# Kernel optimization log

Hardware: AMD Instinct MI355X
Metric: run time of the kernel (lower is better)

## Reference

```python
import jax, jax.numpy as jnp
import numpy as np

N_NODES = 100000
N_EDGES = 1600000
HIDDEN = 128
N_GRAPHS = 64
N_CLASSES = 10


def setup_inputs() -> dict:
    key = jax.random.key(0)
    ks = jax.random.split(key, 10)
    x = jax.random.normal(ks[0], (N_NODES, 1), dtype=jnp.float32)
    edge_index = jax.random.randint(ks[1], (2, N_EDGES), 0, N_NODES, dtype=jnp.int32)
    batch = jnp.sort(jax.random.randint(ks[2], (N_NODES,), 0, N_GRAPHS, dtype=jnp.int32))
    def glorot(k, shape):
        fan_in, fan_out = shape
        s = jnp.sqrt(6.0 / (fan_in + fan_out))
        return jax.random.uniform(k, shape, jnp.float32, -s, s)
    return {
        "x": x,
        "edge_index": edge_index,
        "batch": batch,
        "W1l": glorot(ks[3], (1, HIDDEN)),
        "W1r": glorot(ks[4], (1, HIDDEN)),
        "b1": jnp.zeros((HIDDEN,), jnp.float32),
        "W2l": glorot(ks[5], (HIDDEN, HIDDEN)),
        "W2r": glorot(ks[6], (HIDDEN, HIDDEN)),
        "b2": jnp.zeros((HIDDEN,), jnp.float32),
        "W3l": glorot(ks[7], (HIDDEN, HIDDEN)),
        "W3r": glorot(ks[8], (HIDDEN, HIDDEN)),
        "b3": jnp.zeros((HIDDEN,), jnp.float32),
        "Wfc": glorot(ks[9], (HIDDEN, N_CLASSES)),
        "bfc": jnp.zeros((N_CLASSES,), jnp.float32),
    }


def _sage_conv(x, src, dst, Wl, Wr, b, n_nodes):
    # mean aggregation of source features at destination nodes
    msg = x[src]                                              # [E, d_in]
    agg = jax.ops.segment_sum(msg, dst, num_segments=n_nodes)  # [N, d_in]
    cnt = jax.ops.segment_sum(jnp.ones((src.shape[0], 1), x.dtype), dst,
                              num_segments=n_nodes)            # [N, 1]
    mean = agg / jnp.maximum(cnt, 1.0)
    # PyG SAGEConv: lin_l(mean neighbors) + bias + lin_r(self)
    return mean @ Wl + b + x @ Wr


def reference(x, edge_index, batch, W1l, W1r, b1, W2l, W2r, b2,
              W3l, W3r, b3, Wfc, bfc):
    src, dst = edge_index[0], edge_index[1]
    n = x.shape[0]
    h = jax.nn.relu(_sage_conv(x, src, dst, W1l, W1r, b1, n))
    h = jax.nn.relu(_sage_conv(h, src, dst, W2l, W2r, b2, n))
    h = jax.nn.relu(_sage_conv(h, src, dst, W3l, W3r, b3, n))
    # global_mean_pool over graph ids in `batch`
    pooled = jax.ops.segment_sum(h, batch, num_segments=N_GRAPHS)
    gcnt = jax.ops.segment_sum(jnp.ones((n, 1), h.dtype), batch,
                               num_segments=N_GRAPHS)
    pooled = pooled / jnp.maximum(gcnt, 1.0)
    logits = pooled @ Wfc + bfc
    return jax.nn.log_softmax(logits, axis=1)
```

## Files before the change

kernel.cpp:

```cpp
#include <hip/hip_runtime.h>

typedef unsigned int u32;
typedef unsigned short u16;
typedef short bf16x8 __attribute__((ext_vector_type(8)));
typedef float f32x4 __attribute__((ext_vector_type(4)));
typedef float f32x2 __attribute__((ext_vector_type(2)));
typedef u32 u32x4 __attribute__((ext_vector_type(4)));

#define HBLK 256

__device__ __forceinline__ u16 f2bf(float f) {
  u32 u = __float_as_uint(f);
  u = (u + 0x7FFFu + ((u >> 16) & 1u)) >> 16;
  return (u16)u;
}
__device__ __forceinline__ float bf2f(u32 h) { return __uint_as_float(h << 16); }

__global__ void hist_wprep_kernel(const int* __restrict__ dst, int* __restrict__ hist,
                                  int E, int nbuk, int chunk,
                                  const float* __restrict__ W2l, const float* __restrict__ W2r,
                                  const float* __restrict__ W3l, const float* __restrict__ W3r,
                                  u16* __restrict__ wt2, u16* __restrict__ wt3,
                                  float* __restrict__ pooled, int* __restrict__ gcnt) {
  int idx = blockIdx.x * 256 + threadIdx.x;
  {
    int which = idx >> 15, r = idx & 32767;
    int j = r >> 8, k = r & 255;
    if (which == 0) {
      float v = (k < 128) ? W2l[k * 128 + j] : W2r[(k - 128) * 128 + j];
      wt2[r] = f2bf(v);
    } else {
      float v = (k < 128) ? W3l[k * 128 + j] : W3r[(k - 128) * 128 + j];
      wt3[r] = f2bf(v);
    }
    if (idx < 8192) pooled[idx] = 0.f;
    if (idx < 64) gcnt[idx] = 0;
  }
  __shared__ int h[1024];
  for (int i = threadIdx.x; i < nbuk; i += 256) h[i] = 0;
  __syncthreads();
  int b0 = blockIdx.x * chunk, b1 = min(b0 + chunk, E);
  for (int e = b0 + threadIdx.x; e < b1; e += 256)
    atomicAdd(&h[dst[e] >> 7], 1);
  __syncthreads();
  for (int i = threadIdx.x; i < nbuk; i += 256)
    hist[i * HBLK + blockIdx.x] = h[i];
}

__global__ void scan_local(const int* __restrict__ in, int* __restrict__ out,
                           int* __restrict__ bsum, int n) {
  __shared__ int s[256];
  int tid = threadIdx.x;
  int i = blockIdx.x * 256 + tid;
  int v = (i < n) ? in[i] : 0;
  s[tid] = v;
  __syncthreads();
  for (int off = 1; off < 256; off <<= 1) {
    int t = (tid >= off) ? s[tid - off] : 0;
    __syncthreads();
    s[tid] += t;
    __syncthreads();
  }
  if (i < n) out[i] = s[tid] - v;
  if (tid == 255) bsum[blockIdx.x] = s[255];
}

__global__ void scan_fix(int* __restrict__ a, const int* __restrict__ bsum, int n,
                         int* __restrict__ bbase) {
  __shared__ int red[256];
  int tid = threadIdx.x, b = blockIdx.x;
  int s = 0;
  for (int k = tid; k < b; k += 256) s += bsum[k];
  red[tid] = s;
  __syncthreads();
  for (int off = 128; off; off >>= 1) {
    if (tid < off) red[tid] += red[tid + off];
    __syncthreads();
  }
  int i = b * 256 + tid;
  if (i < n) {
    int v = a[i] + red[0];
    a[i] = v;
    if (tid == 0) bbase[b] = v;
  }
}

__global__ void scatter2_kernel(const int* __restrict__ src, const int* __restrict__ dst,
                                const int* __restrict__ hist_s, u32* __restrict__ part,
                                int E, int nbuk, int chunk) {
  __shared__ int cur[1024];
  for (int i = threadIdx.x; i < nbuk; i += 256)
    cur[i] = hist_s[i * HBLK + blockIdx.x];
  __syncthreads();
  int b0 = blockIdx.x * chunk, b1 = min(b0 + chunk, E);
  for (int e = b0 + threadIdx.x; e < b1; e += 256) {
    int d = dst[e];
    int pos = atomicAdd(&cur[d >> 7], 1);
    part[pos] = (u32)src[e] | ((u32)(d & 127) << 25);
  }
}

__global__ void scatter3_kernel(const u32* __restrict__ part, const int* __restrict__ bbase,
                                const float* __restrict__ x,
                                const float* __restrict__ W1l, const float* __restrict__ W1r,
                                const float* __restrict__ b1,
                                int* __restrict__ roff, int* __restrict__ csr,
                                u32* __restrict__ h1, int E, int nbuk, int n) {
  int b = blockIdx.x;
  int tid = threadIdx.x;
  int base = bbase[b];
  int end = (b + 1 < nbuk) ? bbase[b + 1] : E;
  __shared__ int cnt[128];
  __shared__ int s[128];
  __shared__ int cur[128];
  __shared__ float xsum[128];
  __shared__ float meanv[128];
  __shared__ float wlA[128], wrA[128], bA[128];
  if (tid < 128) {
    cnt[tid] = 0; xsum[tid] = 0.f;
    wlA[tid] = W1l[tid]; wrA[tid] = W1r[tid]; bA[tid] = b1[tid];
  }
  __syncthreads();
  for (int e = base + tid; e < end; e += 256)
    atomicAdd(&cnt[part[e] >> 25], 1);
  __syncthreads();
  if (tid < 128) s[tid] = cnt[tid];
  __syncthreads();
  for (int off = 1; off < 128; off <<= 1) {
    int t = (tid >= off && tid < 128) ? s[tid - off] : 0;
    __syncthreads();
    if (tid < 128) s[tid] += t;
    __syncthreads();
  }
  if (tid < 128) {
    int excl = s[tid] - cnt[tid];
    cur[tid] = base + excl;
    int node = b * 128 + tid;
    if (node < n) roff[node] = base + excl;
  }
  if (b == 0 && tid == 0) roff[n] = E;
  __syncthreads();
  for (int e = base + tid; e < end; e += 256) {
    u32 p = part[e];
    int sidx = (int)(p & 0x1FFFFFFu);
    int pos = atomicAdd(&cur[p >> 25], 1);
    csr[pos] = sidx;
    atomicAdd(&xsum[p >> 25], x[sidx]);
  }
  __syncthreads();
  if (tid < 128) meanv[tid] = xsum[tid] / (float)max(cnt[tid], 1);
  __syncthreads();
  int nlocal = min(128, n - b * 128);
  for (int q = tid; q < nlocal * 64; q += 256) {
    int ln = q >> 6, w = q & 63;
    int node = b * 128 + ln;
    int j0 = w * 2;
    float m = meanv[ln], xs = x[node];
    float v0 = fmaxf(m * wlA[j0] + xs * wrA[j0] + bA[j0], 0.f);
    float v1 = fmaxf(m * wlA[j0 + 1] + xs * wrA[j0 + 1] + bA[j0 + 1], 0.f);
    h1[(size_t)node * 64 + w] = (u32)f2bf(v0) | ((u32)f2bf(v1) << 16);
  }
}

__global__ void agg_kernel(const int* __restrict__ csr, const int* __restrict__ roff,
                           const u32* __restrict__ hin, u32* __restrict__ outv, int n) {
  int wave = threadIdx.x >> 6, lane = threadIdx.x & 63;
  int i = blockIdx.x * 4 + wave;
  if (i >= n) return;
  int grp = lane >> 4, li = lane & 15;
  int e0 = roff[i], e1 = roff[i + 1];
  f32x2 a[4] = {};
  int e = e0 + grp;
  for (; e + 12 < e1; e += 16) {
    int s0 = csr[e], s1 = csr[e + 4], s2 = csr[e + 8], s3 = csr[e + 12];
    u32x4 v0 = *(const u32x4*)(hin + (size_t)s0 * 64 + li * 4);
    u32x4 v1 = *(const u32x4*)(hin + (size_t)s1 * 64 + li * 4);
    u32x4 v2 = *(const u32x4*)(hin + (size_t)s2 * 64 + li * 4);
    u32x4 v3 = *(const u32x4*)(hin + (size_t)s3 * 64 + li * 4);
#pragma unroll
    for (int w = 0; w < 4; ++w) {
      a[w] += (f32x2){bf2f(v0[w] & 0xFFFFu), bf2f(v0[w] >> 16)};
      a[w] += (f32x2){bf2f(v1[w] & 0xFFFFu), bf2f(v1[w] >> 16)};
      a[w] += (f32x2){bf2f(v2[w] & 0xFFFFu), bf2f(v2[w] >> 16)};
      a[w] += (f32x2){bf2f(v3[w] & 0xFFFFu), bf2f(v3[w] >> 16)};
    }
  }
  for (; e + 4 < e1; e += 8) {
    int s0 = csr[e], s1 = csr[e + 4];
    u32x4 v0 = *(const u32x4*)(hin + (size_t)s0 * 64 + li * 4);
    u32x4 v1 = *(const u32x4*)(hin + (size_t)s1 * 64 + li * 4);
#pragma unroll
    for (int w = 0; w < 4; ++w) {
      a[w] += (f32x2){bf2f(v0[w] & 0xFFFFu), bf2f(v0[w] >> 16)};
      a[w] += (f32x2){bf2f(v1[w] & 0xFFFFu), bf2f(v1[w] >> 16)};
    }
  }
  if (e < e1) {
    int s0 = csr[e];
    u32x4 v0 = *(const u32x4*)(hin + (size_t)s0 * 64 + li * 4);
#pragma unroll
    for (int w = 0; w < 4; ++w)
      a[w] += (f32x2){bf2f(v0[w] & 0xFFFFu), bf2f(v0[w] >> 16)};
  }
#pragma unroll
  for (int w = 0; w < 4; ++w) {
    a[w].x += __shfl_xor(a[w].x, 16, 64);
    a[w].y += __shfl_xor(a[w].y, 16, 64);
    a[w].x += __shfl_xor(a[w].x, 32, 64);
    a[w].y += __shfl_xor(a[w].y, 32, 64);
  }
  if (grp == 0) {
    float inv = 1.f / (float)max(e1 - e0, 1);
    u32x4 o;
#pragma unroll
    for (int w = 0; w < 4; ++w)
      o[w] = (u32)f2bf(a[w].x * inv) | ((u32)f2bf(a[w].y * inv) << 16);
    *(u32x4*)(outv + (size_t)i * 64 + li * 4) = o;
  }
}

__launch_bounds__(512)
__global__ void mm_kernel(const u16* Aleft, const u16* Aright,
                          const u16* __restrict__ Wt, const float* __restrict__ bias,
                          u16* Out, int n) {
  __shared__ u16 wlds[32768];
  for (int c = threadIdx.x; c < 4096; c += 512) {
    int j = c >> 5, ch = c & 31;
    int swz = ch ^ (j & 31);
    *(u32x4*)(&wlds[j * 256 + swz * 8]) = *(const u32x4*)(&Wt[j * 256 + ch * 8]);
  }
  __syncthreads();
  int wave = threadIdx.x >> 6;
  int lane = threadIdx.x & 63;
  int quad = lane >> 4, l16 = lane & 15;
  int row0 = blockIdx.x * 128 + wave * 16;
  int m = row0 + l16;
  int mc = m < n ? m : (n - 1);
  f32x4 acc[8] = {};
  const u16* Ah[2] = {Aleft, Aright};
#pragma unroll
  for (int half = 0; half < 2; ++half) {
    const u16* A = Ah[half] + (size_t)mc * 128;
#pragma unroll
    for (int s = 0; s < 4; ++s) {
      bf16x8 a = *(const bf16x8*)(A + s * 32 + quad * 8);
      int chunk = (half << 4) + (s << 2) + quad;
#pragma unroll
      for (int t = 0; t < 8; ++t) {
        int j = t * 16 + l16;
        int swz = chunk ^ (j & 31);
        bf16x8 b = *(const bf16x8*)(&wlds[j * 256 + swz * 8]);
        acc[t] = __builtin_amdgcn_mfma_f32_16x16x32_bf16(a, b, acc[t], 0, 0, 0);
      }
    }
  }
#pragma unroll
  for (int t = 0; t < 8; ++t) {
    int j = t * 16 + l16;
    float bj = bias[j];
#pragma unroll
    for (int r = 0; r < 4; ++r) {
      int mr = row0 + quad * 4 + r;
      if (mr < n) {
        float v = acc[t][r] + bj;
        Out[(size_t)mr * 128 + j] = f2bf(fmaxf(v, 0.f));
      }
    }
  }
}

#define PB_NODES 128
__global__ void pool_partial(const int* __restrict__ batch, const u32* __restrict__ h3,
                             float* __restrict__ pooled, int* __restrict__ gcnt, int n) {
  __shared__ int bg[PB_NODES];
  int tid = threadIdx.x;
  int start = blockIdx.x * PB_NODES;
  int cntN = min(PB_NODES, n - start);
  if (tid < cntN) bg[tid] = batch[start + tid];
  __syncthreads();
  int wave = tid >> 6, lane = tid & 63;
  float a0 = 0.f, a1 = 0.f;
  int gcur = -1, cnt = 0;
  int k = wave;
  for (; k + 12 < cntN; k += 16) {
    u32 v0 = h3[(size_t)(start + k) * 64 + lane];
    u32 v1 = h3[(size_t)(start + k + 4) * 64 + lane];
    u32 v2 = h3[(size_t)(start + k + 8) * 64 + lane];
    u32 v3 = h3[(size_t)(start + k + 12) * 64 + lane];
    int g0 = bg[k], g1 = bg[k + 4], g2 = bg[k + 8], g3 = bg[k + 12];
    u32 vv[4] = {v0, v1, v2, v3};
    int gg[4] = {g0, g1, g2, g3};
#pragma unroll
    for (int q = 0; q < 4; ++q) {
      if (gg[q] != gcur) {
        if (gcur >= 0) {
          atomicAdd(&pooled[gcur * 128 + lane * 2], a0);
          atomicAdd(&pooled[gcur * 128 + lane * 2 + 1], a1);
          if (lane == 0) atomicAdd(&gcnt[gcur], cnt);
        }
        gcur = gg[q]; a0 = 0.f; a1 = 0.f; cnt = 0;
      }
      a0 += bf2f(vv[q] & 0xFFFFu);
      a1 += bf2f(vv[q] >> 16);
      cnt++;
    }
  }
  for (; k < cntN; k += 4) {
    u32 v = h3[(size_t)(start + k) * 64 + lane];
    int g = bg[k];
    if (g != gcur) {
      if (gcur >= 0) {
        atomicAdd(&pooled[gcur * 128 + lane * 2], a0);
        atomicAdd(&pooled[gcur * 128 + lane * 2 + 1], a1);
        if (lane == 0) atomicAdd(&gcnt[gcur], cnt);
      }
      gcur = g; a0 = 0.f; a1 = 0.f; cnt = 0;
    }
    a0 += bf2f(v & 0xFFFFu);
    a1 += bf2f(v >> 16);
    cnt++;
  }
  if (gcur >= 0) {
    atomicAdd(&pooled[gcur * 128 + lane * 2], a0);
    atomicAdd(&pooled[gcur * 128 + lane * 2 + 1], a1);
    if (lane == 0) atomicAdd(&gcnt[gcur], cnt);
  }
}

__global__ void head_kernel(const float* __restrict__ pooled, const int* __restrict__ gcnt,
                            const float* __restrict__ Wfc, const float* __restrict__ bfc,
                            float* __restrict__ out) {
  __shared__ float lg[64][10];
  int t = threadIdx.x;
  if (t < 640) {
    int g = t / 10, c = t % 10;
    float inv = 1.f / (float)max(gcnt[g], 1);
    float acc = bfc[c];
    for (int k = 0; k < 128; ++k) acc += pooled[g * 128 + k] * inv * Wfc[k * 10 + c];
    lg[g][c] = acc;
  }
  __syncthreads();
  if (t < 640) {
    int g = t / 10, c = t % 10;
    float mx = -1e30f;
    for (int q = 0; q < 10; ++q) mx = fmaxf(mx, lg[g][q]);
    float se = 0.f;
    for (int q = 0; q < 10; ++q) se += expf(lg[g][q] - mx);
    out[g * 10 + c] = lg[g][c] - mx - logf(se);
  }
}

extern "C" void kernel_launch(void* const* d_in, const int* in_sizes, int n_in,
                              void* d_out, int out_size, void* d_ws, size_t ws_size,
                              hipStream_t stream) {
  const float* x   = (const float*)d_in[0];
  const int* ei    = (const int*)d_in[1];
  const int* batch = (const int*)d_in[2];
  const float* W1l = (const float*)d_in[3];
  const float* W1r = (const float*)d_in[4];
  const float* b1  = (const float*)d_in[5];
  const float* W2l = (const float*)d_in[6];
  const float* W2r = (const float*)d_in[7];
  const float* b2  = (const float*)d_in[8];
  const float* W3l = (const float*)d_in[9];
  const float* W3r = (const float*)d_in[10];
  const float* b3  = (const float*)d_in[11];
  const float* Wfc = (const float*)d_in[12];
  const float* bfc = (const float*)d_in[13];
  float* out = (float*)d_out;
  int N = in_sizes[0];
  int E = in_sizes[1] / 2;
  const int* src = ei;
  const int* dst = ei + E;

  char* p = (char*)d_ws;
  auto alloc = [&](size_t bytes) { void* r = (void*)p; p += (bytes + 255) & ~(size_t)255; return r; };
  int* roff   = (int*)alloc((size_t)(N + 1) * 4);
  int* csr    = (int*)alloc((size_t)E * 4);
  u32* bufA   = (u32*)alloc((size_t)N * 64 * 4);
  u32* bufB   = (u32*)alloc((size_t)N * 64 * 4);
  u16* wt2    = (u16*)alloc(32768 * 2);
  u16* wt3    = (u16*)alloc(32768 * 2);
  float* pooled = (float*)alloc(64 * 128 * 4);
  int* gcnt   = (int*)alloc(64 * 4);
  int* bsum   = (int*)alloc(1024 * 4);
  int* bbase  = (int*)alloc(1024 * 4);

  int nbuk = (N + 127) >> 7;
  int* hist = (int*)bufA;
  u32* part = (u32*)bufB;
  int chunk = (E + HBLK - 1) / HBLK;
  int nH = nbuk * HBLK;
  int nbH = (nH + 255) / 256;

  hist_wprep_kernel<<<HBLK, 256, 0, stream>>>(dst, hist, E, nbuk, chunk,
                                              W2l, W2r, W3l, W3r, wt2, wt3,
                                              pooled, gcnt);
  scan_local<<<nbH, 256, 0, stream>>>(hist, hist, bsum, nH);
  scan_fix<<<nbH, 256, 0, stream>>>(hist, bsum, nH, bbase);
  scatter2_kernel<<<HBLK, 256, 0, stream>>>(src, dst, hist, part, E, nbuk, chunk);
  scatter3_kernel<<<nbuk, 256, 0, stream>>>(part, bbase, x, W1l, W1r, b1,
                                            roff, csr, bufA, E, nbuk, N);
  agg_kernel<<<(N + 3) / 4, 256, 0, stream>>>(csr, roff, bufA, bufB, N);
  mm_kernel<<<(N + 127) / 128, 512, 0, stream>>>((const u16*)bufB, (const u16*)bufA, wt2, b2, (u16*)bufB, N);
  agg_kernel<<<(N + 3) / 4, 256, 0, stream>>>(csr, roff, bufB, bufA, N);
  mm_kernel<<<(N + 127) / 128, 512, 0, stream>>>((const u16*)bufA, (const u16*)bufB, wt3, b3, (u16*)bufA, N);
  pool_partial<<<(N + PB_NODES - 1) / PB_NODES, 256, 0, stream>>>(batch, bufA, pooled, gcnt, N);
  head_kernel<<<1, 640, 0, stream>>>(pooled, gcnt, Wfc, bfc, out);
}
```

Measured before the change: 346.0 us.

## Replace scan kernels with atomic bucket offsets and fuse pooling into final matmul

The two-pass global scan over the per-block histogram is removed. Each block now claims its bucket offset with an atomicAdd on per-bucket totals, and scatter2 computes the exclusive scan over the roughly 800 bucket totals itself in shared memory. The mean-pool partial reduction moves into the tail of the last mm_kernel, which reads back its freshly written output tile. This cuts three launches and one extra pass over h3, in exchange for a memset, a nondeterministic edge order inside each bucket, and a pooling loop that is no longer unrolled.

New measurement: 359.8 us. 1.04x slower.

```diff
diff --git a/kernel.cpp b/kernel.cpp
--- a/kernel.cpp
+++ b/kernel.cpp
@@ -16,8 +16,8 @@
 }
 __device__ __forceinline__ float bf2f(u32 h) { return __uint_as_float(h << 16); }
 
-__global__ void hist_wprep_kernel(const int* __restrict__ dst, int* __restrict__ hist,
-                                  int E, int nbuk, int chunk,
+__global__ void hist_wprep_kernel(const int* __restrict__ dst, int* __restrict__ boff,
+                                  int* __restrict__ btotal, int E, int nbuk, int chunk,
                                   const float* __restrict__ W2l, const float* __restrict__ W2r,
                                   const float* __restrict__ W3l, const float* __restrict__ W3r,
                                   u16* __restrict__ wt2, u16* __restrict__ wt3,
@@ -44,56 +44,44 @@
     atomicAdd(&h[dst[e] >> 7], 1);
   __syncthreads();
   for (int i = threadIdx.x; i < nbuk; i += 256)
-    hist[i * HBLK + blockIdx.x] = h[i];
-}
-
-__global__ void scan_local(const int* __restrict__ in, int* __restrict__ out,
-                           int* __restrict__ bsum, int n) {
-  __shared__ int s[256];
+    boff[i * HBLK + blockIdx.x] = atomicAdd(&btotal[i], h[i]);
+}
+
+__global__ void scatter2_kernel(const int* __restrict__ src, const int* __restrict__ dst,
+                                const int* __restrict__ btotal, const int* __restrict__ boff,
+                                u32* __restrict__ part, int* __restrict__ bbase,
+                                int E, int nbuk, int chunk) {
+  __shared__ int bt[1024];
+  __shared__ int wsum[256];
+  __shared__ int cur[1024];
   int tid = threadIdx.x;
-  int i = blockIdx.x * 256 + tid;
-  int v = (i < n) ? in[i] : 0;
-  s[tid] = v;
+  int t4 = tid * 4;
+  int v0 = (t4 + 0 < nbuk) ? btotal[t4 + 0] : 0;
+  int v1 = (t4 + 1 < nbuk) ? btotal[t4 + 1] : 0;
+  int v2 = (t4 + 2 < nbuk) ? btotal[t4 + 2] : 0;
+  int v3 = (t4 + 3 < nbuk) ? btotal[t4 + 3] : 0;
+  int sum = v0 + v1 + v2 + v3;
+  wsum[tid] = sum;
   __syncthreads();
   for (int off = 1; off < 256; off <<= 1) {
-    int t = (tid >= off) ? s[tid - off] : 0;
+    int t = (tid >= off) ? wsum[tid - off] : 0;
     __syncthreads();
-    s[tid] += t;
+    wsum[tid] += t;
     __syncthreads();
   }
-  if (i < n) out[i] = s[tid] - v;
-  if (tid == 255) bsum[blockIdx.x] = s[255];
-}
-
-__global__ void scan_fix(int* __restrict__ a, const int* __restrict__ bsum, int n,
-                         int* __restrict__ bbase) {
-  __shared__ int red[256];
-  int tid = threadIdx.x, b = blockIdx.x;
-  int s = 0;
-  for (int k = tid; k < b; k += 256) s += bsum[k];
-  red[tid] = s;
-  __syncthreads();
-  for (int off = 128; off; off >>= 1) {
-    if (tid < off) red[tid] += red[tid + off];
-    __syncthreads();
-  }
-  int i = b * 256 + tid;
-  if (i < n) {
-    int v = a[i] + red[0];
-    a[i] = v;
-    if (tid == 0) bbase[b] = v;
-  }
-}
-
-__global__ void scatter2_kernel(const int* __restrict__ src, const int* __restrict__ dst,
-                                const int* __restrict__ hist_s, u32* __restrict__ part,
-                                int E, int nbuk, int chunk) {
-  __shared__ int cur[1024];
-  for (int i = threadIdx.x; i < nbuk; i += 256)
-    cur[i] = hist_s[i * HBLK + blockIdx.x];
+  int excl = wsum[tid] - sum;
+  bt[t4 + 0] = excl;
+  bt[t4 + 1] = excl + v0;
+  bt[t4 + 2] = excl + v0 + v1;
+  bt[t4 + 3] = excl + v0 + v1 + v2;
+  __syncthreads();
+  for (int i = tid; i < nbuk; i += 256) {
+    cur[i] = bt[i] + boff[i * HBLK + blockIdx.x];
+    if (blockIdx.x == 0) bbase[i] = bt[i];
+  }
   __syncthreads();
   int b0 = blockIdx.x * chunk, b1 = min(b0 + chunk, E);
-  for (int e = b0 + threadIdx.x; e < b1; e += 256) {
+  for (int e = b0 + tid; e < b1; e += 256) {
     int d = dst[e];
     int pos = atomicAdd(&cur[d >> 7], 1);
     part[pos] = (u32)src[e] | ((u32)(d & 127) << 25);
@@ -222,8 +210,11 @@
 __launch_bounds__(512)
 __global__ void mm_kernel(const u16* Aleft, const u16* Aright,
                           const u16* __restrict__ Wt, const float* __restrict__ bias,
-                          u16* Out, int n) {
+                          u16* Out, int n,
+                          const int* __restrict__ batch, float* __restrict__ pooled,
+                          int* __restrict__ gcnt, int doPool) {
   __shared__ u16 wlds[32768];
+  __shared__ int bg[128];
   for (int c = threadIdx.x; c < 4096; c += 512) {
     int j = c >> 5, ch = c & 31;
     int swz = ch ^ (j & 31);
@@ -267,46 +258,17 @@
       }
     }
   }
-}
-
-#define PB_NODES 128
-__global__ void pool_partial(const int* __restrict__ batch, const u32* __restrict__ h3,
-                             float* __restrict__ pooled, int* __restrict__ gcnt, int n) {
-  __shared__ int bg[PB_NODES];
-  int tid = threadIdx.x;
-  int start = blockIdx.x * PB_NODES;
-  int cntN = min(PB_NODES, n - start);
-  if (tid < cntN) bg[tid] = batch[start + tid];
-  __syncthreads();
-  int wave = tid >> 6, lane = tid & 63;
+  if (!doPool) return;
+  __syncthreads();
+  int start = blockIdx.x * 128;
+  int cntN = min(128, n - start);
+  if (threadIdx.x < cntN) bg[threadIdx.x] = batch[start + threadIdx.x];
+  __syncthreads();
+  const u32* O32 = (const u32*)Out;
   float a0 = 0.f, a1 = 0.f;
   int gcur = -1, cnt = 0;
-  int k = wave;
-  for (; k + 12 < cntN; k += 16) {
-    u32 v0 = h3[(size_t)(start + k) * 64 + lane];
-    u32 v1 = h3[(size_t)(start + k + 4) * 64 + lane];
-    u32 v2 = h3[(size_t)(start + k + 8) * 64 + lane];
-    u32 v3 = h3[(size_t)(start + k + 12) * 64 + lane];
-    int g0 = bg[k], g1 = bg[k + 4], g2 = bg[k + 8], g3 = bg[k + 12];
-    u32 vv[4] = {v0, v1, v2, v3};
-    int gg[4] = {g0, g1, g2, g3};
-#pragma unroll
-    for (int q = 0; q < 4; ++q) {
-      if (gg[q] != gcur) {
-        if (gcur >= 0) {
-          atomicAdd(&pooled[gcur * 128 + lane * 2], a0);
-          atomicAdd(&pooled[gcur * 128 + lane * 2 + 1], a1);
-          if (lane == 0) atomicAdd(&gcnt[gcur], cnt);
-        }
-        gcur = gg[q]; a0 = 0.f; a1 = 0.f; cnt = 0;
-      }
-      a0 += bf2f(vv[q] & 0xFFFFu);
-      a1 += bf2f(vv[q] >> 16);
-      cnt++;
-    }
-  }
-  for (; k < cntN; k += 4) {
-    u32 v = h3[(size_t)(start + k) * 64 + lane];
+  for (int k = wave; k < cntN; k += 8) {
+    u32 v = O32[(size_t)(start + k) * 64 + lane];
     int g = bg[k];
     if (g != gcur) {
       if (gcur >= 0) {
@@ -383,28 +345,27 @@
   u16* wt3    = (u16*)alloc(32768 * 2);
   float* pooled = (float*)alloc(64 * 128 * 4);
   int* gcnt   = (int*)alloc(64 * 4);
-  int* bsum   = (int*)alloc(1024 * 4);
+  int* btotal = (int*)alloc(1024 * 4);
   int* bbase  = (int*)alloc(1024 * 4);
 
   int nbuk = (N + 127) >> 7;
-  int* hist = (int*)bufA;
+  int* boff = (int*)bufA;
   u32* part = (u32*)bufB;
   int chunk = (E + HBLK - 1) / HBLK;
-  int nH = nbuk * HBLK;
-  int nbH = (nH + 255) / 256;
-
-  hist_wprep_kernel<<<HBLK, 256, 0, stream>>>(dst, hist, E, nbuk, chunk,
+
+  hipMemsetAsync(btotal, 0, 1024 * 4, stream);
+  hist_wprep_kernel<<<HBLK, 256, 0, stream>>>(dst, boff, btotal, E, nbuk, chunk,
                                               W2l, W2r, W3l, W3r, wt2, wt3,
                                               pooled, gcnt);
-  scan_local<<<nbH, 256, 0, stream>>>(hist, hist, bsum, nH);
-  scan_fix<<<nbH, 256, 0, stream>>>(hist, bsum, nH, bbase);
-  scatter2_kernel<<<HBLK, 256, 0, stream>>>(src, dst, hist, part, E, nbuk, chunk);
+  scatter2_kernel<<<HBLK, 256, 0, stream>>>(src, dst, btotal, boff, part, bbase,
+                                            E, nbuk, chunk);
   scatter3_kernel<<<nbuk, 256, 0, stream>>>(part, bbase, x, W1l, W1r, b1,
                                             roff, csr, bufA, E, nbuk, N);
   agg_kernel<<<(N + 3) / 4, 256, 0, stream>>>(csr, roff, bufA, bufB, N);
-  mm_kernel<<<(N + 127) / 128, 512, 0, stream>>>((const u16*)bufB, (const u16*)bufA, wt2, b2, (u16*)bufB, N);
+  mm_kernel<<<(N + 127) / 128, 512, 0, stream>>>((const u16*)bufB, (const u16*)bufA, wt2, b2,
+                                                 (u16*)bufB, N, batch, pooled, gcnt, 0);
   agg_kernel<<<(N + 3) / 4, 256, 0, stream>>>(csr, roff, bufB, bufA, N);
-  mm_kernel<<<(N + 127) / 128, 512, 0, stream>>>((const u16*)bufA, (const u16*)bufB, wt3, b3, (u16*)bufA, N);
-  pool_partial<<<(N + PB_NODES - 1) / PB_NODES, 256, 0, stream>>>(batch, bufA, pooled, gcnt, N);
+  mm_kernel<<<(N + 127) / 128, 512, 0, stream>>>((const u16*)bufA, (const u16*)bufB, wt3, b3,
+                                                 (u16*)bufA, N, batch, pooled, gcnt, 1);
   head_kernel<<<1, 640, 0, stream>>>(pooled, gcnt, Wfc, bfc, out);
 }
```
